# Kernel tuning notes

Hardware: AMD Instinct MI355X
Metric: run time of the kernel (lower is better)

## Reference

```python
import jax, jax.numpy as jnp
import numpy as np

D = 1024        # d_group
H = 8           # num_heads_group
WIN = 128       # attention window size
DH = D // H     # head_dim = 128
EPS = 1e-5


def _rmsnorm(x, scale):
    xf = x.astype(jnp.float32)
    var = jnp.mean(jnp.square(xf), axis=-1, keepdims=True)
    return (xf * jax.lax.rsqrt(var + EPS) * scale.astype(jnp.float32)).astype(x.dtype)


def _rope(x):
    # x: [B', S, H, Dh]
    S, Dh = x.shape[1], x.shape[3]
    freqs = 1.0 / (10000.0 ** (jnp.arange(0, Dh, 2, dtype=jnp.float32) / Dh))
    ang = jnp.arange(S, dtype=jnp.float32)[:, None] * freqs[None, :]  # [S, Dh/2]
    sin = jnp.repeat(jnp.sin(ang), 2, axis=-1)[None, :, None, :]
    cos = jnp.repeat(jnp.cos(ang), 2, axis=-1)[None, :, None, :]
    x1, x2 = jnp.split(x, 2, axis=-1)
    rot = jnp.concatenate([-x2, x1], axis=-1)
    return x * cos + rot * sin


def setup_inputs() -> dict:
    key = jax.random.key(0)
    ks = jax.random.split(key, 16)
    s = 0.02
    return {
        "group_x": jax.random.normal(ks[0], (8, 4096, D), jnp.float32),
        "context": jax.random.normal(ks[1], (8, D), jnp.float32),
        "W_ada": jax.random.normal(ks[2], (D, 6 * D), jnp.float32) * s,
        "b_ada": jnp.zeros((6 * D,), jnp.float32),
        "scale1": jnp.ones((D,), jnp.float32),
        "W_qkv": jax.random.normal(ks[3], (D, 3 * D), jnp.float32) * s,
        "b_qkv": jnp.zeros((3 * D,), jnp.float32),
        "W_out": jax.random.normal(ks[4], (D, D), jnp.float32) * s,
        "b_out": jnp.zeros((D,), jnp.float32),
        "scale2": jnp.ones((D,), jnp.float32),
        "W_ff1": jax.random.normal(ks[5], (D, 4 * D), jnp.float32) * s,
        "b_ff1": jnp.zeros((4 * D,), jnp.float32),
        "W_ff2": jax.random.normal(ks[6], (4 * D, D), jnp.float32) * s,
        "b_ff2": jnp.zeros((D,), jnp.float32),
    }


def reference(group_x, context, W_ada, b_ada, scale1, W_qkv, b_qkv, W_out, b_out,
              scale2, W_ff1, b_ff1, W_ff2, b_ff2):
    B, L, _ = group_x.shape
    nw = L // WIN

    # adaLN modulation params from context
    ada = jax.nn.silu(context) @ W_ada + b_ada              # [B, 6D]
    sh_msa, sc_msa, g_msa, sh_mlp, sc_mlp, g_mlp = jnp.split(ada, 6, axis=-1)
    sh_msa, sc_msa, g_msa = sh_msa[:, None], sc_msa[:, None], g_msa[:, None]
    sh_mlp, sc_mlp, g_mlp = sh_mlp[:, None], sc_mlp[:, None], g_mlp[:, None]

    # --- attention branch ---
    res = group_x
    x = _rmsnorm(group_x, scale1)
    x = x * (1 + sc_msa) + sh_msa
    xw = x.reshape(B * nw, WIN, D)
    qkv = xw @ W_qkv + b_qkv
    q, k, v = jnp.split(qkv, 3, axis=-1)
    q = _rope(q.reshape(B * nw, WIN, H, DH))
    k = _rope(k.reshape(B * nw, WIN, H, DH))
    v = v.reshape(B * nw, WIN, H, DH)
    scores = jnp.einsum('bqhd,bkhd->bhqk', q, k) / jnp.sqrt(jnp.float32(DH))
    attn = jax.nn.softmax(scores, axis=-1)
    o = jnp.einsum('bhqk,bkhd->bqhd', attn, v).reshape(B, L, D)
    o = o @ W_out + b_out
    x = res + g_msa * o

    # --- MLP branch ---
    res = x
    h = _rmsnorm(x, scale2)
    h = h * (1 + sc_mlp) + sh_mlp
    h = jax.nn.gelu(h @ W_ff1 + b_ff1)
    h = h @ W_ff2 + b_ff2
    return res + g_mlp * h
```

## Files before the change

kernel.cpp:

```cpp
#include <hip/hip_runtime.h>
#include <cstdint>
#include <cstddef>

typedef __bf16 bf16;
typedef __bf16 bf16x2 __attribute__((ext_vector_type(2)));
typedef __bf16 bf16x4 __attribute__((ext_vector_type(4)));
typedef __bf16 bf16x8 __attribute__((ext_vector_type(8)));
typedef float f32x4 __attribute__((ext_vector_type(4)));

#define D_MODEL 1024
#define ADA_STRIDE 6144
#define ROWS_TOTAL 32768
#define EPS_RMS 1e-5f

__device__ __forceinline__ void gld16(const void* g, void* l) {
  __builtin_amdgcn_global_load_lds((const __attribute__((address_space(1))) void*)g,
                                   (__attribute__((address_space(3))) void*)l, 16, 0, 0);
}

__global__ void wconvert_t(const float* __restrict__ W, bf16* __restrict__ Wt,
                           int kbits, int N, int total) {
  int i = blockIdx.x * 256 + threadIdx.x;
  if (i >= total) return;
  int K = 1 << kbits;
  int k = i & (K - 1);
  int n = i >> kbits;
  Wt[i] = (bf16)W[(size_t)k * N + n];
}

__global__ void ada_gemm(const float* __restrict__ ctx, const float* __restrict__ W,
                         const float* __restrict__ bias, float* __restrict__ ada) {
  __shared__ float sc[D_MODEL];
  int b = blockIdx.y;
  int col = blockIdx.x * 256 + threadIdx.x;
  for (int j = threadIdx.x; j < D_MODEL; j += 256) {
    float x = ctx[b * D_MODEL + j];
    sc[j] = x / (1.f + __expf(-x));
  }
  __syncthreads();
  float acc = bias[col];
#pragma unroll 8
  for (int k = 0; k < D_MODEL; ++k)
    acc += sc[k] * W[(size_t)k * ADA_STRIDE + col];
  ada[b * ADA_STRIDE + col] = acc;
}

__global__ void rmsnorm_mod(const float* __restrict__ x, const float* __restrict__ scale,
                            const float* __restrict__ ada, int shOff, int scOff,
                            bf16* __restrict__ out) {
  int row = blockIdx.x;
  int b = row >> 12;
  int t = threadIdx.x;
  const float* xr = x + (size_t)row * D_MODEL;
  float4 v = ((const float4*)xr)[t];
  float ss = v.x * v.x + v.y * v.y + v.z * v.z + v.w * v.w;
#pragma unroll
  for (int m = 32; m >= 1; m >>= 1) ss += __shfl_xor(ss, m, 64);
  __shared__ float ws[4];
  if ((t & 63) == 0) ws[t >> 6] = ss;
  __syncthreads();
  float tot = ws[0] + ws[1] + ws[2] + ws[3];
  float rms = rsqrtf(tot * (1.f / D_MODEL) + EPS_RMS);
  const float* ab = ada + b * ADA_STRIDE;
  int d0 = t * 4;
  float vv[4] = {v.x, v.y, v.z, v.w};
  bf16x4 o4;
#pragma unroll
  for (int j = 0; j < 4; ++j) {
    int d = d0 + j;
    float y = vv[j] * rms * scale[d];
    y = y * (1.f + ab[scOff + d]) + ab[shOff + d];
    o4[j] = (bf16)y;
  }
  *(bf16x4*)(out + (size_t)row * D_MODEL + d0) = o4;
}

__global__ void rope_kernel(bf16* __restrict__ qk) {
  int gid = blockIdx.x * 256 + threadIdx.x;
  int t = gid >> 5, i = gid & 31;
  int pos = t & 127;
  float fl = __expf((float)i * -0.14391156831f);
  float al = (float)pos * fl, ah = al * 0.01f;
  float sl, cl, sh, ch;
  __sincosf(al, &sl, &cl);
  __sincosf(ah, &sh, &ch);
  bf16* row = qk + (size_t)t * 2048;
  int d0 = i * 2;
#pragma unroll
  for (int h8 = 0; h8 < 16; ++h8) {
    bf16* hp = row + h8 * 128;
    bf16x2 lo = *(bf16x2*)(hp + d0);
    bf16x2 hi = *(bf16x2*)(hp + 64 + d0);
    bf16x2 olo, ohi;
#pragma unroll
    for (int j = 0; j < 2; ++j) {
      float xl = (float)lo[j], xh = (float)hi[j];
      olo[j] = (bf16)(xl * cl - xh * sl);
      ohi[j] = (bf16)(xh * ch + xl * sh);
    }
    *(bf16x2*)(hp + d0) = olo;
    *(bf16x2*)(hp + 64 + d0) = ohi;
  }
}

#define GEMM_LDS 131072

struct Frags {
  bf16x8 a[8];
  bf16x8 b[4];
};

__device__ __forceinline__ void load_frags(const bf16* lds, int slot, int aBase, int bBase, Frags& f) {
  const bf16* sa = lds + slot * 16384 + aBase;
  const bf16* sb = lds + slot * 16384 + bBase;
#pragma unroll
  for (int mi = 0; mi < 8; ++mi) f.a[mi] = *(const bf16x8*)(sa + mi * 512);
#pragma unroll
  for (int ni = 0; ni < 4; ++ni) f.b[ni] = *(const bf16x8*)(sb + ni * 512);
}

__device__ __forceinline__ void do_mfma(const Frags& f, f32x4 (&acc)[8][4]) {
  __builtin_amdgcn_s_setprio(1);
#pragma unroll
  for (int mi = 0; mi < 8; ++mi)
#pragma unroll
    for (int ni = 0; ni < 4; ++ni)
      acc[mi][ni] = __builtin_amdgcn_mfma_f32_16x16x32_bf16(f.b[ni], f.a[mi], acc[mi][ni], 0, 0, 0);
  __builtin_amdgcn_s_setprio(0);
}

#define VMWAIT(N) asm volatile("s_waitcnt vmcnt(" #N ")" ::: "memory")

template <int EPI>
__global__ __launch_bounds__(512, 2) void gemm256(
    const bf16* __restrict__ A, const bf16* __restrict__ Bt,
    const float* __restrict__ bias, int M, int K, int N,
    bf16* __restrict__ outB, float* __restrict__ outF,
    const float* __restrict__ resid, const float* __restrict__ ada, int gOff) {
  extern __shared__ char smem_raw[];
  bf16* lds = (bf16*)smem_raw;
  const int tid = threadIdx.x;
  const int lane = tid & 63;
  const int wv = tid >> 6;
  const int wm = wv >> 2;
  const int wn = wv & 3;
  const int lm = lane & 15;
  const int quad = lane >> 4;
  const int px = quad ^ ((lm >> 2) & 3);

  const int MT = M >> 8, NT = N >> 8;
  const int nwg = MT * NT;
  const int bid = blockIdx.x;
  const int wgid = (bid & 7) * (nwg >> 3) + (bid >> 3);
  const int width = 8 * NT;
  const int gid = wgid / width;
  const int first = gid * 8;
  const int gsize = (MT - first < 8) ? (MT - first) : 8;
  const int inG = wgid % width;
  const int tileM = (first + inG % gsize) << 8;
  const int tileN = (inG / gsize) << 8;

  const int sr = tid >> 2;
  const int sg = tid & 3;
  const int gl = sg ^ ((sr >> 2) & 3);
  const bf16* gA0 = A + (size_t)(tileM + sr) * K + gl * 8;
  const bf16* gA1 = gA0 + (size_t)128 * K;
  const bf16* gB0 = Bt + (size_t)(tileN + sr) * K + gl * 8;
  const bf16* gB1 = gB0 + (size_t)128 * K;
  bf16* lw = lds + tid * 8;

#define STAGE256(T) { \
    bf16* l = lw + ((T) & 3) * 16384; \
    const size_t ko = (size_t)(T) * 32; \
    gld16(gA0 + ko, l); \
    gld16(gA1 + ko, l + 4096); \
    gld16(gB0 + ko, l + 8192); \
    gld16(gB1 + ko, l + 12288); }

  f32x4 acc[8][4];
#pragma unroll
  for (int mi = 0; mi < 8; ++mi)
#pragma unroll
    for (int ni = 0; ni < 4; ++ni) acc[mi][ni] = (f32x4){0.f, 0.f, 0.f, 0.f};

  const int aBase = (wm * 128 + lm) * 32 + px * 8;
  const int bBase = 8192 + (wn * 64 + lm) * 32 + px * 8;

  STAGE256(0);
  STAGE256(1);
  STAGE256(2);

  const int nt = K >> 5;
  Frags f;
  int t = 0;
  for (; t < nt - 3; ++t) {
    VMWAIT(8);
    __builtin_amdgcn_s_barrier();
    load_frags(lds, t & 3, aBase, bBase, f);
    STAGE256(t + 3);
    do_mfma(f, acc);
  }
  VMWAIT(8);
  __builtin_amdgcn_s_barrier();
  load_frags(lds, t & 3, aBase, bBase, f);
  do_mfma(f, acc);
  ++t;
  VMWAIT(4);
  __builtin_amdgcn_s_barrier();
  load_frags(lds, t & 3, aBase, bBase, f);
  do_mfma(f, acc);
  ++t;
  VMWAIT(0);
  __builtin_amdgcn_s_barrier();
  load_frags(lds, t & 3, aBase, bBase, f);
  do_mfma(f, acc);

#pragma unroll
  for (int mi = 0; mi < 8; ++mi) {
    int grow = tileM + wm * 128 + mi * 16 + lm;
    int b = grow >> 12;
    float brow = (EPI == 4) ? bias[grow] : 0.f;
#pragma unroll
    for (int ni = 0; ni < 4; ++ni) {
      int col0 = tileN + wn * 64 + ni * 16 + quad * 4;
      size_t idx = (size_t)grow * N + col0;
      if (EPI == 0) {
        float4 b4 = *(const float4*)(bias + col0);
        float bb[4] = {b4.x, b4.y, b4.z, b4.w};
        bf16x4 o;
#pragma unroll
        for (int r = 0; r < 4; ++r) o[r] = (bf16)(acc[mi][ni][r] + bb[r]);
        *(bf16x4*)(outB + idx) = o;
      } else if (EPI == 4) {
        bf16x4 o;
#pragma unroll
        for (int r = 0; r < 4; ++r) o[r] = (bf16)(acc[mi][ni][r] + brow);
        *(bf16x4*)(outB + idx) = o;
      } else if (EPI == 1) {
        float4 b4 = *(const float4*)(bias + col0);
        float bb[4] = {b4.x, b4.y, b4.z, b4.w};
        bf16x4 o;
#pragma unroll
        for (int r = 0; r < 4; ++r) {
          float v = acc[mi][ni][r] + bb[r];
          float s2 = 1.5957691216057308f * (v + 0.044715f * v * v * v);
          o[r] = (bf16)(v / (1.f + __expf(-s2)));
        }
        *(bf16x4*)(outB + idx) = o;
      } else if (EPI == 2) {
        float4 b4 = *(const float4*)(bias + col0);
        float4 g4 = *(const float4*)(ada + b * ADA_STRIDE + gOff + col0);
        float4 r4 = *(const float4*)(resid + idx);
        float4 o4;
        o4.x = r4.x + g4.x * (acc[mi][ni][0] + b4.x);
        o4.y = r4.y + g4.y * (acc[mi][ni][1] + b4.y);
        o4.z = r4.z + g4.z * (acc[mi][ni][2] + b4.z);
        o4.w = r4.w + g4.w * (acc[mi][ni][3] + b4.w);
        *(float4*)(outF + idx) = o4;
      } else {
        float4 b4 = *(const float4*)(bias + col0);
        float4 g4 = *(const float4*)(ada + b * ADA_STRIDE + gOff + col0);
        float4 r4 = *(const float4*)(outF + idx);
        float4 o4;
        o4.x = r4.x + g4.x * (acc[mi][ni][0] + b4.x);
        o4.y = r4.y + g4.y * (acc[mi][ni][1] + b4.y);
        o4.z = r4.z + g4.z * (acc[mi][ni][2] + b4.z);
        o4.w = r4.w + g4.w * (acc[mi][ni][3] + b4.w);
        *(float4*)(outF + idx) = o4;
      }
    }
  }
}

#define ATTN_LDS 65536

__global__ __launch_bounds__(256, 2) void attn_kernel(
    const bf16* __restrict__ qk, const bf16* __restrict__ vt, bf16* __restrict__ o) {
  extern __shared__ char smem[];
  bf16* qbuf = (bf16*)smem;
  bf16* kbuf = qbuf + 128 * 128;
  const int tid = threadIdx.x;
  const int lane = tid & 63;
  const int wv = tid >> 6;
  const int lm = lane & 15;
  const int quad = lane >> 4;
  const int w = blockIdx.x >> 3;
  const int h = blockIdx.x & 7;
  const int wbase = w * 128;

#pragma unroll
  for (int it = 0; it < 8; ++it) {
    int c = it * 256 + tid;
    int r = c >> 4, gst = c & 15;
    int goff = (gst ^ (r & 15)) * 8;
    const bf16* rowp = qk + (size_t)(wbase + r) * 2048 + h * 128 + goff;
    gld16(rowp, qbuf + c * 8);
    gld16(rowp + 1024, kbuf + c * 8);
  }
  __syncthreads();

  const int wq0 = wv * 32;
  f32x4 accS[8][2];
#pragma unroll
  for (int mi = 0; mi < 8; ++mi)
#pragma unroll
    for (int ni = 0; ni < 2; ++ni) accS[mi][ni] = (f32x4){0.f, 0.f, 0.f, 0.f};

#pragma unroll
  for (int s = 0; s < 4; ++s) {
    bf16x8 bq[2], ak[8];
#pragma unroll
    for (int ni = 0; ni < 2; ++ni)
      bq[ni] = *(const bf16x8*)(qbuf + (wq0 + ni * 16 + lm) * 128 + ((s * 4 + quad) ^ lm) * 8);
#pragma unroll
    for (int mi = 0; mi < 8; ++mi)
      ak[mi] = *(const bf16x8*)(kbuf + (mi * 16 + lm) * 128 + ((s * 4 + quad) ^ lm) * 8);
#pragma unroll
    for (int mi = 0; mi < 8; ++mi)
#pragma unroll
      for (int ni = 0; ni < 2; ++ni)
        accS[mi][ni] = __builtin_amdgcn_mfma_f32_16x16x32_bf16(ak[mi], bq[ni], accS[mi][ni], 0, 0, 0);
  }

  const float scl = 0.08838834764831845f;
  float mx[2] = {-1e30f, -1e30f}, sm[2] = {0.f, 0.f};
#pragma unroll
  for (int mi = 0; mi < 8; ++mi)
#pragma unroll
    for (int ni = 0; ni < 2; ++ni)
#pragma unroll
      for (int r = 0; r < 4; ++r) {
        accS[mi][ni][r] *= scl;
        mx[ni] = fmaxf(mx[ni], accS[mi][ni][r]);
      }
#pragma unroll
  for (int ni = 0; ni < 2; ++ni) {
    mx[ni] = fmaxf(mx[ni], __shfl_xor(mx[ni], 16, 64));
    mx[ni] = fmaxf(mx[ni], __shfl_xor(mx[ni], 32, 64));
  }
#pragma unroll
  for (int mi = 0; mi < 8; ++mi)
#pragma unroll
    for (int ni = 0; ni < 2; ++ni)
#pragma unroll
      for (int r = 0; r < 4; ++r) {
        accS[mi][ni][r] = __expf(accS[mi][ni][r] - mx[ni]);
        sm[ni] += accS[mi][ni][r];
      }
#pragma unroll
  for (int ni = 0; ni < 2; ++ni) {
    sm[ni] += __shfl_xor(sm[ni], 16, 64);
    sm[ni] += __shfl_xor(sm[ni], 32, 64);
    sm[ni] = 1.f / sm[ni];
  }
  __syncthreads();

#pragma unroll
  for (int mi = 0; mi < 8; ++mi)
#pragma unroll
    for (int ni = 0; ni < 2; ++ni) {
      int q = wq0 + ni * 16 + lm;
      int gst = (mi * 2 + (quad >> 1)) ^ lm;
      bf16x4 pk;
#pragma unroll
      for (int r = 0; r < 4; ++r) pk[r] = (bf16)(accS[mi][ni][r] * sm[ni]);
      *(bf16x4*)(qbuf + q * 128 + gst * 8 + (quad & 1) * 4) = pk;
    }
#pragma unroll
  for (int it = 0; it < 8; ++it) {
    int c = it * 256 + tid;
    int r = c >> 4, gst = c & 15;
    gld16(vt + (size_t)(h * 128 + r) * 32768 + wbase + (gst ^ (r & 15)) * 8, kbuf + c * 8);
  }
  __syncthreads();

  f32x4 accO[2][8];
#pragma unroll
  for (int mi = 0; mi < 2; ++mi)
#pragma unroll
    for (int ni = 0; ni < 8; ++ni) accO[mi][ni] = (f32x4){0.f, 0.f, 0.f, 0.f};
#pragma unroll
  for (int s = 0; s < 4; ++s) {
    bf16x8 ap[2], bv[8];
#pragma unroll
    for (int mi = 0; mi < 2; ++mi)
      ap[mi] = *(const bf16x8*)(qbuf + (wq0 + mi * 16 + lm) * 128 + ((s * 4 + quad) ^ lm) * 8);
#pragma unroll
    for (int ni = 0; ni < 8; ++ni)
      bv[ni] = *(const bf16x8*)(kbuf + (ni * 16 + lm) * 128 + ((s * 4 + quad) ^ lm) * 8);
#pragma unroll
    for (int mi = 0; mi < 2; ++mi)
#pragma unroll
      for (int ni = 0; ni < 8; ++ni)
        accO[mi][ni] = __builtin_amdgcn_mfma_f32_16x16x32_bf16(ap[mi], bv[ni], accO[mi][ni], 0, 0, 0);
  }

#pragma unroll
  for (int mi = 0; mi < 2; ++mi)
#pragma unroll
    for (int ni = 0; ni < 8; ++ni) {
      int d = ni * 16 + lm;
#pragma unroll
      for (int r = 0; r < 4; ++r) {
        int q = wq0 + mi * 16 + quad * 4 + r;
        o[(size_t)(wbase + q) * 1024 + h * 128 + d] = (bf16)accO[mi][ni][r];
      }
    }
}

extern "C" void kernel_launch(void* const* d_in, const int* in_sizes, int n_in,
                              void* d_out, int out_size, void* d_ws, size_t ws_size,
                              hipStream_t stream) {
  const float* group_x = (const float*)d_in[0];
  const float* context = (const float*)d_in[1];
  const float* W_ada   = (const float*)d_in[2];
  const float* b_ada   = (const float*)d_in[3];
  const float* scale1  = (const float*)d_in[4];
  const float* W_qkv   = (const float*)d_in[5];
  const float* b_qkv   = (const float*)d_in[6];
  const float* W_out   = (const float*)d_in[7];
  const float* b_out   = (const float*)d_in[8];
  const float* scale2  = (const float*)d_in[9];
  const float* W_ff1   = (const float*)d_in[10];
  const float* b_ff1   = (const float*)d_in[11];
  const float* W_ff2   = (const float*)d_in[12];
  const float* b_ff2   = (const float*)d_in[13];
  float* out = (float*)d_out;

  char* ws = (char*)d_ws;
  float* ada   = (float*)ws;
  bf16* wqkv_t = (bf16*)(ws + 196608);
  bf16* wout_t = wqkv_t + (size_t)3072 * 1024;
  bf16* wff1_t = wout_t + (size_t)1024 * 1024;
  bf16* wff2_t = wff1_t + (size_t)4096 * 1024;
  bf16* bufX   = wff2_t + (size_t)1024 * 4096;
  bf16* qkvQK  = bufX + (size_t)ROWS_TOTAL * 1024;
  bf16* vtbuf  = qkvQK + (size_t)ROWS_TOTAL * 2048;
  bf16* h1     = qkvQK;

  wconvert_t<<<dim3(3072 * 1024 / 256), 256, 0, stream>>>(W_qkv, wqkv_t, 10, 3072, 3072 * 1024);
  wconvert_t<<<dim3(1024 * 1024 / 256), 256, 0, stream>>>(W_out, wout_t, 10, 1024, 1024 * 1024);
  wconvert_t<<<dim3(4096 * 1024 / 256), 256, 0, stream>>>(W_ff1, wff1_t, 10, 4096, 4096 * 1024);
  wconvert_t<<<dim3(1024 * 4096 / 256), 256, 0, stream>>>(W_ff2, wff2_t, 12, 1024, 1024 * 4096);

  ada_gemm<<<dim3(ADA_STRIDE / 256, 8), 256, 0, stream>>>(context, W_ada, b_ada, ada);

  rmsnorm_mod<<<ROWS_TOTAL, 256, 0, stream>>>(group_x, scale1, ada, 0, 1024, bufX);

  hipFuncSetAttribute(reinterpret_cast<const void*>(&gemm256<0>),
                      hipFuncAttributeMaxDynamicSharedMemorySize, GEMM_LDS);
  hipFuncSetAttribute(reinterpret_cast<const void*>(&gemm256<1>),
                      hipFuncAttributeMaxDynamicSharedMemorySize, GEMM_LDS);
  hipFuncSetAttribute(reinterpret_cast<const void*>(&gemm256<2>),
                      hipFuncAttributeMaxDynamicSharedMemorySize, GEMM_LDS);
  hipFuncSetAttribute(reinterpret_cast<const void*>(&gemm256<3>),
                      hipFuncAttributeMaxDynamicSharedMemorySize, GEMM_LDS);
  hipFuncSetAttribute(reinterpret_cast<const void*>(&gemm256<4>),
                      hipFuncAttributeMaxDynamicSharedMemorySize, GEMM_LDS);

  gemm256<0><<<dim3(128 * 8), 512, GEMM_LDS, stream>>>(
      bufX, wqkv_t, b_qkv, ROWS_TOTAL, 1024, 2048, qkvQK, nullptr, nullptr, nullptr, 0);

  gemm256<4><<<dim3(4 * 128), 512, GEMM_LDS, stream>>>(
      wqkv_t + (size_t)2048 * 1024, bufX, b_qkv + 2048, 1024, 1024, ROWS_TOTAL,
      vtbuf, nullptr, nullptr, nullptr, 0);

  rope_kernel<<<dim3(ROWS_TOTAL * 32 / 256), 256, 0, stream>>>(qkvQK);

  hipFuncSetAttribute(reinterpret_cast<const void*>(&attn_kernel),
                      hipFuncAttributeMaxDynamicSharedMemorySize, ATTN_LDS);
  attn_kernel<<<dim3(256 * 8), 256, ATTN_LDS, stream>>>(qkvQK, vtbuf, bufX);

  gemm256<2><<<dim3(128 * 4), 512, GEMM_LDS, stream>>>(
      bufX, wout_t, b_out, ROWS_TOTAL, 1024, 1024, nullptr, out, group_x, ada, 2048);

  rmsnorm_mod<<<ROWS_TOTAL, 256, 0, stream>>>(out, scale2, ada, 3072, 4096, bufX);

  gemm256<1><<<dim3(128 * 16), 512, GEMM_LDS, stream>>>(
      bufX, wff1_t, b_ff1, ROWS_TOTAL, 1024, 4096, h1, nullptr, nullptr, nullptr, 0);

  gemm256<3><<<dim3(128 * 4), 512, GEMM_LDS, stream>>>(
      h1, wff2_t, b_ff2, ROWS_TOTAL, 4096, 1024, nullptr, out, nullptr, ada, 5120);
}
```

Measured before the change: 1.501 ms.

## Restructure GEMM mainloop into 64-wide K tiles with four-phase interleaved loads

Replaces the 4-slot, 32-wide K pipeline with a double-buffered 64-wide K tile. Each tile is split into four phases, and each phase issues its fragment reads, the next tile's global-to-LDS loads and one quarter of the MFMAs, with barriers between phases. The LDS layout changes to 64-element rows with an 8-way XOR swizzle. The aim is finer overlap of memory traffic with MFMA work and fewer register-held fragments, at the cost of more barriers per tile and more delicate vmcnt accounting.

```diff
diff --git a/kernel.cpp b/kernel.cpp
--- a/kernel.cpp
+++ b/kernel.cpp
@@ -105,31 +105,49 @@
 
 #define GEMM_LDS 131072
 
-struct Frags {
-  bf16x8 a[8];
-  bf16x8 b[4];
-};
-
-__device__ __forceinline__ void load_frags(const bf16* lds, int slot, int aBase, int bBase, Frags& f) {
-  const bf16* sa = lds + slot * 16384 + aBase;
-  const bf16* sb = lds + slot * 16384 + bBase;
-#pragma unroll
-  for (int mi = 0; mi < 8; ++mi) f.a[mi] = *(const bf16x8*)(sa + mi * 512);
-#pragma unroll
-  for (int ni = 0; ni < 4; ++ni) f.b[ni] = *(const bf16x8*)(sb + ni * 512);
-}
-
-__device__ __forceinline__ void do_mfma(const Frags& f, f32x4 (&acc)[8][4]) {
-  __builtin_amdgcn_s_setprio(1);
-#pragma unroll
-  for (int mi = 0; mi < 8; ++mi)
-#pragma unroll
-    for (int ni = 0; ni < 4; ++ni)
-      acc[mi][ni] = __builtin_amdgcn_mfma_f32_16x16x32_bf16(f.b[ni], f.a[mi], acc[mi][ni], 0, 0, 0);
-  __builtin_amdgcn_s_setprio(0);
-}
-
 #define VMWAIT(N) asm volatile("s_waitcnt vmcnt(" #N ")" ::: "memory")
+#define PH_BAR() __builtin_amdgcn_s_barrier()
+#define KT_DO(...) __VA_ARGS__
+#define KT_SKIP(...)
+
+#define READ_AE() { _Pragma("unroll") for (int m_ = 0; m_ < 4; ++m_) \
+  _Pragma("unroll") for (int s_ = 0; s_ < 2; ++s_) \
+    a[m_][s_] = *(const bf16x8*)(lds + cb + aRow + m_ * 2048 + (g0 ^ (s_ * 32))); }
+#define READ_AO() { _Pragma("unroll") for (int m_ = 0; m_ < 4; ++m_) \
+  _Pragma("unroll") for (int s_ = 0; s_ < 2; ++s_) \
+    a[m_][s_] = *(const bf16x8*)(lds + cb + aRow + 1024 + m_ * 2048 + (g0 ^ (s_ * 32))); }
+#define READ_BE() { _Pragma("unroll") for (int n_ = 0; n_ < 2; ++n_) \
+  _Pragma("unroll") for (int s_ = 0; s_ < 2; ++s_) \
+    be[n_][s_] = *(const bf16x8*)(lds + cb + bRow + n_ * 2048 + (g0 ^ (s_ * 32))); }
+#define READ_BO() { _Pragma("unroll") for (int n_ = 0; n_ < 2; ++n_) \
+  _Pragma("unroll") for (int s_ = 0; s_ < 2; ++s_) \
+    bo[n_][s_] = *(const bf16x8*)(lds + cb + bRow + 1024 + n_ * 2048 + (g0 ^ (s_ * 32))); }
+
+#define MMPH(MOFF, BREG, NOFF) { __builtin_amdgcn_s_setprio(1); \
+  _Pragma("unroll") for (int m_ = 0; m_ < 4; ++m_) \
+  _Pragma("unroll") for (int n_ = 0; n_ < 2; ++n_) \
+  _Pragma("unroll") for (int s_ = 0; s_ < 2; ++s_) \
+    acc[2 * m_ + (MOFF)][2 * n_ + (NOFF)] = __builtin_amdgcn_mfma_f32_16x16x32_bf16( \
+        BREG[n_][s_], a[m_][s_], acc[2 * m_ + (MOFF)][2 * n_ + (NOFF)], 0, 0, 0); \
+  __builtin_amdgcn_s_setprio(0); }
+
+#define KTILE(W0, W1, W2, STG) { \
+    VMWAIT(W0); PH_BAR(); \
+    READ_AE(); READ_BE(); \
+    STG(gld16(gA + ko2, ldAn); gld16(gA + ko2 + K8, ldAn + 512);) \
+    MMPH(0, be, 0); \
+    VMWAIT(W1); PH_BAR(); \
+    READ_BO(); \
+    STG(gld16(gB + ko2, ldBn); gld16(gB + ko2 + K8, ldBn + 512);) \
+    MMPH(0, bo, 1); \
+    VMWAIT(W2); PH_BAR(); \
+    READ_AO(); \
+    STG(gld16(gB + ko2 + K16, ldBn + 1024); gld16(gB + ko2 + K24, ldBn + 1536);) \
+    MMPH(1, bo, 1); \
+    PH_BAR(); \
+    STG(gld16(gA + ko2 + K16, ldAn + 1024); gld16(gA + ko2 + K24, ldAn + 1536);) \
+    MMPH(1, be, 0); \
+  }
 
 template <int EPI>
 __global__ __launch_bounds__(512, 2) void gemm256(
@@ -146,7 +164,6 @@
   const int wn = wv & 3;
   const int lm = lane & 15;
   const int quad = lane >> 4;
-  const int px = quad ^ ((lm >> 2) & 3);
 
   const int MT = M >> 8, NT = N >> 8;
   const int nwg = MT * NT;
@@ -160,60 +177,42 @@
   const int tileM = (first + inG % gsize) << 8;
   const int tileN = (inG / gsize) << 8;
 
-  const int sr = tid >> 2;
-  const int sg = tid & 3;
-  const int gl = sg ^ ((sr >> 2) & 3);
-  const bf16* gA0 = A + (size_t)(tileM + sr) * K + gl * 8;
-  const bf16* gA1 = gA0 + (size_t)128 * K;
-  const bf16* gB0 = Bt + (size_t)(tileN + sr) * K + gl * 8;
-  const bf16* gB1 = gB0 + (size_t)128 * K;
-  bf16* lw = lds + tid * 8;
-
-#define STAGE256(T) { \
-    bf16* l = lw + ((T) & 3) * 16384; \
-    const size_t ko = (size_t)(T) * 32; \
-    gld16(gA0 + ko, l); \
-    gld16(gA1 + ko, l + 4096); \
-    gld16(gB0 + ko, l + 8192); \
-    gld16(gB1 + ko, l + 12288); }
+  const int srow = 32 * (tid >> 6) + ((tid & 63) >> 3);
+  const int xg = ((tid & 7) ^ ((tid >> 3) & 7)) * 8;
+  const bf16* gA = A + (size_t)(tileM + srow) * K + xg;
+  const bf16* gB = Bt + (size_t)(tileN + srow) * K + xg;
+  const size_t K8 = (size_t)K * 8;
+  const size_t K16 = K8 * 2, K24 = K8 * 3;
+  bf16* ldA = lds + (tid >> 6) * 2048 + (tid & 63) * 8;
+  bf16* ldB = ldA + 16384;
 
   f32x4 acc[8][4];
 #pragma unroll
-  for (int mi = 0; mi < 8; ++mi)
-#pragma unroll
-    for (int ni = 0; ni < 4; ++ni) acc[mi][ni] = (f32x4){0.f, 0.f, 0.f, 0.f};
-
-  const int aBase = (wm * 128 + lm) * 32 + px * 8;
-  const int bBase = 8192 + (wn * 64 + lm) * 32 + px * 8;
-
-  STAGE256(0);
-  STAGE256(1);
-  STAGE256(2);
-
-  const int nt = K >> 5;
-  Frags f;
-  int t = 0;
-  for (; t < nt - 3; ++t) {
-    VMWAIT(8);
-    __builtin_amdgcn_s_barrier();
-    load_frags(lds, t & 3, aBase, bBase, f);
-    STAGE256(t + 3);
-    do_mfma(f, acc);
-  }
-  VMWAIT(8);
-  __builtin_amdgcn_s_barrier();
-  load_frags(lds, t & 3, aBase, bBase, f);
-  do_mfma(f, acc);
-  ++t;
-  VMWAIT(4);
-  __builtin_amdgcn_s_barrier();
-  load_frags(lds, t & 3, aBase, bBase, f);
-  do_mfma(f, acc);
-  ++t;
-  VMWAIT(0);
-  __builtin_amdgcn_s_barrier();
-  load_frags(lds, t & 3, aBase, bBase, f);
-  do_mfma(f, acc);
+  for (int i = 0; i < 8; ++i)
+#pragma unroll
+    for (int j = 0; j < 4; ++j) acc[i][j] = (f32x4){0.f, 0.f, 0.f, 0.f};
+
+  const int g0 = (quad ^ (lm & 7)) * 8;
+  const int aRow = wm * 8192 + lm * 64;
+  const int bRow = 16384 + wn * 4096 + lm * 64;
+
+  bf16x8 a[4][2], be[2][2], bo[2][2];
+
+  gld16(gA, ldA);        gld16(gA + K8, ldA + 512);
+  gld16(gB, ldB);        gld16(gB + K8, ldB + 512);
+  gld16(gB + K16, ldB + 1024); gld16(gB + K24, ldB + 1536);
+  gld16(gA + K16, ldA + 1024); gld16(gA + K24, ldA + 1536);
+
+  const int nt = K >> 6;
+  int cb = 0;
+  for (int t = 0; t < nt - 1; ++t) {
+    bf16* ldAn = ldA + (cb ^ 32768);
+    bf16* ldBn = ldB + (cb ^ 32768);
+    const size_t ko2 = (size_t)(t + 1) * 64;
+    KTILE(4, 4, 4, KT_DO)
+    cb ^= 32768;
+  }
+  KTILE(4, 2, 0, KT_SKIP)
 
 #pragma unroll
   for (int mi = 0; mi < 8; ++mi) {
```

Result: faster. 1.424 ms (-5.1%).
